# Performance work log

Hardware: AMD Instinct MI355X
Metric: run time of the kernel (lower is better)

The kernel has to match this reference:

```python
import jax, jax.numpy as jnp
import numpy as np

N = 100000      # nodes
E = 1600000     # edges (before self-loops)
IN_DIM = 128
HEADS = 4
C = 32          # hid_dim // heads = 128 // 4
SLOPE = 0.2     # PyG GATConv default negative_slope


def setup_inputs() -> dict:
    key = jax.random.key(0)
    k1, k2, k3, k4, k5 = jax.random.split(key, 5)
    x = jax.random.normal(k1, (N, IN_DIM), dtype=jnp.float32)
    edge_index = jax.random.randint(k2, (2, E), 0, N, dtype=jnp.int32)
    # learned parameters of GATConv
    W = jax.random.normal(k3, (IN_DIM, HEADS * C), dtype=jnp.float32) / np.sqrt(IN_DIM)
    att_src = jax.random.normal(k4, (HEADS, C), dtype=jnp.float32) * 0.1
    att_dst = jax.random.normal(k5, (HEADS, C), dtype=jnp.float32) * 0.1
    bias = jnp.zeros((HEADS * C,), dtype=jnp.float32)
    return {"x": x, "edge_index": edge_index, "W": W,
            "att_src": att_src, "att_dst": att_dst, "bias": bias}


def reference(x, edge_index, W, att_src, att_dst, bias):
    # PyG GATConv default add_self_loops=True
    loops = jnp.arange(N, dtype=edge_index.dtype)
    ei = jnp.concatenate([edge_index, jnp.stack([loops, loops])], axis=1)
    src, dst = ei[0], ei[1]                       # messages flow src -> dst

    h = (x @ W).reshape(N, HEADS, C)              # [N,H,C]
    a_src = jnp.einsum('nhc,hc->nh', h, att_src)  # [N,H]
    a_dst = jnp.einsum('nhc,hc->nh', h, att_dst)  # [N,H]

    e = a_src[src] + a_dst[dst]                   # [E+N,H] per-edge logits
    e = jax.nn.leaky_relu(e, SLOPE)

    # segment softmax over edges sharing a destination node
    m = jax.ops.segment_max(e, dst, num_segments=N)        # [N,H]
    e = jnp.exp(e - m[dst])
    s = jax.ops.segment_sum(e, dst, num_segments=N)        # [N,H]
    alpha = e / (s[dst] + 1e-16)                            # [E+N,H]

    msg = h[src] * alpha[:, :, None]                        # [E+N,H,C]
    out = jax.ops.segment_sum(msg, dst, num_segments=N)     # [N,H,C]
    return out.reshape(N, HEADS * C) + bias                 # concat heads + bias
```

## Files before the change

### kernel.cpp

```cpp
#include <hip/hip_runtime.h>
#include <cstddef>

#define HEADS 4
#define HC 128
#define SLOPE 0.2f
#define NPBUCK 256
#define NSBMAX 512
#define SBCAP 5120
#define CHUNK 4096

using half8 = __attribute__((ext_vector_type(8))) _Float16;
using f32x4 = __attribute__((ext_vector_type(4))) float;

__device__ __forceinline__ float edge_w(float v) {
    v = v > 0.f ? v : SLOPE * v;
    return __expf(v);
}
__device__ __forceinline__ float2 up2(unsigned w) {
    union { unsigned u; _Float16 f[2]; } c; c.u = w;
    return make_float2((float)c.f[0], (float)c.f[1]);
}

__global__ void wt_kernel(const float* __restrict__ W, _Float16* __restrict__ WTh) {
    int k = threadIdx.x;
    int nn = blockIdx.x;
    WTh[nn * HC + k] = (_Float16)W[k * HC + nn];
}

__global__ __launch_bounds__(256)
void gemm_att_count_kernel(const float* __restrict__ x, const _Float16* __restrict__ WTh,
                           const float* __restrict__ att_src, const float* __restrict__ att_dst,
                           _Float16* __restrict__ h2,
                           float* __restrict__ a_s, float* __restrict__ a_d,
                           const int* __restrict__ ei, int* __restrict__ cnt2d,
                           int gb, int E, int n) {
    __shared__ int cnt[NSBMAX];
    int tid = threadIdx.x;

    if (blockIdx.x >= gb) {
        int cb = blockIdx.x - gb;
        for (int i = tid; i < NSBMAX; i += 256) cnt[i] = 0;
        __syncthreads();
        int Etot = E + n;
        int e0 = cb * CHUNK;
        int eend = e0 + CHUNK; if (eend > Etot) eend = Etot;
        for (int e = e0 + tid; e < eend; e += 256) {
            int dst = (e < E) ? ei[E + e] : (e - E);
            atomicAdd(&cnt[dst >> 8], 1);
        }
        __syncthreads();
        int* row = cnt2d + (size_t)cb * NSBMAX;
        for (int i = tid; i < NSBMAX; i += 256) row[i] = cnt[i];
        return;
    }

    int wv   = tid >> 6;
    int lane = tid & 63;
    int t    = lane & 15;
    int q    = lane >> 4;
    int r0   = blockIdx.x * 64 + wv * 16;

    f32x4 acc[8];
#pragma unroll
    for (int ct = 0; ct < 8; ++ct) acc[ct] = (f32x4){0.f, 0.f, 0.f, 0.f};

    int  arow = r0 + t;
    bool aval = arow < n;
    const float* xp = x + (size_t)(aval ? arow : 0) * HC;

    for (int kc = 0; kc < 4; ++kc) {
        int k0 = kc * 32 + q * 8;
        half8 a;
        float4 fa = *(const float4*)(xp + k0);
        float4 fb = *(const float4*)(xp + k0 + 4);
        if (!aval) { fa = make_float4(0.f,0.f,0.f,0.f); fb = fa; }
        a[0] = (_Float16)fa.x; a[1] = (_Float16)fa.y;
        a[2] = (_Float16)fa.z; a[3] = (_Float16)fa.w;
        a[4] = (_Float16)fb.x; a[5] = (_Float16)fb.y;
        a[6] = (_Float16)fb.z; a[7] = (_Float16)fb.w;
#pragma unroll
        for (int ct = 0; ct < 8; ++ct) {
            half8 b = *(const half8*)(WTh + (size_t)(ct * 16 + t) * HC + k0);
            acc[ct] = __builtin_amdgcn_mfma_f32_16x16x32_f16(a, b, acc[ct], 0, 0, 0);
        }
    }

#pragma unroll
    for (int reg = 0; reg < 4; ++reg) {
        int row = r0 + q * 4 + reg;
        if (row < n) {
#pragma unroll
            for (int ct = 0; ct < 8; ++ct)
                h2[(size_t)row * HC + ct * 16 + t] = (_Float16)acc[ct][reg];
        }
    }

    float asv[8], adv[8];
#pragma unroll
    for (int ct = 0; ct < 8; ++ct) {
        asv[ct] = att_src[ct * 16 + t];
        adv[ct] = att_dst[ct * 16 + t];
    }
#pragma unroll
    for (int reg = 0; reg < 4; ++reg) {
        int row = r0 + q * 4 + reg;
        float4 ps, pd;
        ps.x = acc[0][reg]*asv[0] + acc[1][reg]*asv[1];
        ps.y = acc[2][reg]*asv[2] + acc[3][reg]*asv[3];
        ps.z = acc[4][reg]*asv[4] + acc[5][reg]*asv[5];
        ps.w = acc[6][reg]*asv[6] + acc[7][reg]*asv[7];
        pd.x = acc[0][reg]*adv[0] + acc[1][reg]*adv[1];
        pd.y = acc[2][reg]*adv[2] + acc[3][reg]*adv[3];
        pd.z = acc[4][reg]*adv[4] + acc[5][reg]*adv[5];
        pd.w = acc[6][reg]*adv[6] + acc[7][reg]*adv[7];
#pragma unroll
        for (int m = 1; m < 16; m <<= 1) {
            ps.x += __shfl_xor(ps.x, m); ps.y += __shfl_xor(ps.y, m);
            ps.z += __shfl_xor(ps.z, m); ps.w += __shfl_xor(ps.w, m);
            pd.x += __shfl_xor(pd.x, m); pd.y += __shfl_xor(pd.y, m);
            pd.z += __shfl_xor(pd.z, m); pd.w += __shfl_xor(pd.w, m);
        }
        if (t == 0 && row < n) {
            ((float4*)a_s)[row] = ps;
            ((float4*)a_d)[row] = pd;
        }
    }
}

__global__ __launch_bounds__(512)
void colscan_kernel(const int* __restrict__ cnt2d, int* __restrict__ base2d,
                    int* __restrict__ bucketend, int nchunks) {
    __shared__ int tmp[512];
    int b = blockIdx.x;
    int t = threadIdx.x;
    int v = (t < nchunks) ? cnt2d[(size_t)t * NSBMAX + b] : 0;
    tmp[t] = v;
    __syncthreads();
#pragma unroll
    for (int off = 1; off < 512; off <<= 1) {
        int u = (t >= off) ? tmp[t - off] : 0;
        __syncthreads();
        tmp[t] += u;
        __syncthreads();
    }
    if (t < nchunks) base2d[(size_t)t * NSBMAX + b] = b * SBCAP + tmp[t] - v;
    if (t == 511) bucketend[b] = b * SBCAP + tmp[511];
}

__global__ __launch_bounds__(256)
void scatter_kernel(const int* __restrict__ ei, int E, int n,
                    const int* __restrict__ base2d, int2* __restrict__ binned) {
    __shared__ int cur[NSBMAX];
    int tid = threadIdx.x;
    const int* row = base2d + (size_t)blockIdx.x * NSBMAX;
    for (int i = tid; i < NSBMAX; i += 256) cur[i] = row[i];
    __syncthreads();
    int Etot = E + n;
    int e0 = blockIdx.x * CHUNK;
    int eend = e0 + CHUNK; if (eend > Etot) eend = Etot;
    for (int e = e0 + tid; e < eend; e += 256) {
        int src, dst;
        if (e < E) { src = ei[e]; dst = ei[E + e]; }
        else       { src = e - E; dst = src; }
        int p = atomicAdd(&cur[dst >> 8], 1);
        binned[p] = make_int2(src, dst);
    }
}

__global__ __launch_bounds__(256)
void place_kernel(const int* __restrict__ bucketend, const int2* __restrict__ binned,
                  int* __restrict__ sorted, int* __restrict__ rowstart,
                  int* __restrict__ deg, int n) {
    __shared__ int cnt[256];
    __shared__ int pos[256];
    int b = blockIdx.x;
    int dst0 = b << 8;
    int rows = n - dst0; if (rows > 256) rows = 256;
    int tid = threadIdx.x;

    cnt[tid] = 0;
    __syncthreads();
    int wstart = b * SBCAP;
    int wend   = bucketend[b];
    for (int e = wstart + tid; e < wend; e += 256)
        atomicAdd(&cnt[binned[e].y - dst0], 1);
    __syncthreads();

    int d = cnt[tid];
    pos[tid] = d;
    __syncthreads();
#pragma unroll
    for (int off = 1; off < 256; off <<= 1) {
        int v = (tid >= off) ? pos[tid - off] : 0;
        __syncthreads();
        pos[tid] += v;
        __syncthreads();
    }
    int excl = pos[tid] - d;
    if (tid < rows) {
        rowstart[dst0 + tid] = wstart + excl;
        deg[dst0 + tid] = d;
    }
    cnt[tid] = excl;
    __syncthreads();
    for (int e = wstart + tid; e < wend; e += 256) {
        int2 ed = binned[e];
        int p = atomicAdd(&cnt[ed.y - dst0], 1);
        sorted[wstart + p] = ed.x;
    }
}

__global__ __launch_bounds__(256)
void agg_kernel(const int* __restrict__ rowstart, const int* __restrict__ deg,
                const int* __restrict__ sorted,
                const float* __restrict__ a_s, const float* __restrict__ a_d,
                const _Float16* __restrict__ h2, const float* __restrict__ bias,
                float* __restrict__ out, int n) {
    int dst = blockIdx.x * 4 + (threadIdx.x >> 6);
    if (dst >= n) return;
    int lane = threadIdx.x & 63;
    int li   = lane & 15;
    int sub  = lane >> 4;
    int head = li >> 2;
    int start = rowstart[dst];
    int cntv  = deg[dst];

    float ad = a_d[(size_t)dst * 4 + head];
    const uint4* h4 = (const uint4*)h2;
    float acc[8] = {0.f,0.f,0.f,0.f,0.f,0.f,0.f,0.f};
    float wsum = 0.f;

    for (int j = 0; j < cntv; j += 16) {
        int   sv[4]; float wv[4]; uint4 hv[4];
#pragma unroll
        for (int k = 0; k < 4; ++k) {
            int idx = j + k * 4 + sub;
            bool valid = idx < cntv;
            sv[k] = sorted[start + (valid ? idx : cntv - 1)];
            wv[k] = valid ? 1.f : 0.f;
        }
#pragma unroll
        for (int k = 0; k < 4; ++k)
            hv[k] = h4[(size_t)sv[k] * 16 + li];
#pragma unroll
        for (int k = 0; k < 4; ++k) {
            float w = wv[k] * edge_w(a_s[(size_t)sv[k] * 4 + head] + ad);
            float2 f0 = up2(hv[k].x), f1 = up2(hv[k].y),
                   f2 = up2(hv[k].z), f3 = up2(hv[k].w);
            acc[0] = fmaf(w, f0.x, acc[0]); acc[1] = fmaf(w, f0.y, acc[1]);
            acc[2] = fmaf(w, f1.x, acc[2]); acc[3] = fmaf(w, f1.y, acc[3]);
            acc[4] = fmaf(w, f2.x, acc[4]); acc[5] = fmaf(w, f2.y, acc[5]);
            acc[6] = fmaf(w, f3.x, acc[6]); acc[7] = fmaf(w, f3.y, acc[7]);
            wsum += w;
        }
    }

#pragma unroll
    for (int k = 0; k < 8; ++k) {
        acc[k] += __shfl_xor(acc[k], 16);
        acc[k] += __shfl_xor(acc[k], 32);
    }
    wsum += __shfl_xor(wsum, 16);
    wsum += __shfl_xor(wsum, 32);

    if (sub == 0) {
        float inv = 1.f / wsum;
        float4 b0 = ((const float4*)bias)[li * 2];
        float4 b1 = ((const float4*)bias)[li * 2 + 1];
        float4 o0 = make_float4(acc[0]*inv + b0.x, acc[1]*inv + b0.y,
                                acc[2]*inv + b0.z, acc[3]*inv + b0.w);
        float4 o1 = make_float4(acc[4]*inv + b1.x, acc[5]*inv + b1.y,
                                acc[6]*inv + b1.z, acc[7]*inv + b1.w);
        float4* op = (float4*)(out + (size_t)dst * HC);
        op[li * 2]     = o0;
        op[li * 2 + 1] = o1;
    }
}

extern "C" void kernel_launch(void* const* d_in, const int* in_sizes, int n_in,
                              void* d_out, int out_size, void* d_ws, size_t ws_size,
                              hipStream_t stream) {
    const float* x       = (const float*)d_in[0];
    const int*   ei      = (const int*)d_in[1];
    const float* W       = (const float*)d_in[2];
    const float* att_src = (const float*)d_in[3];
    const float* att_dst = (const float*)d_in[4];
    const float* bias    = (const float*)d_in[5];

    int n = in_sizes[0] / HC;
    int E = in_sizes[1] / 2;
    int Etot = E + n;
    int nbuck   = (n + NPBUCK - 1) / NPBUCK;
    int nchunks = (Etot + CHUNK - 1) / CHUNK;
    int gb      = (n + 63) / 64;

    _Float16* h2     = (_Float16*)d_ws;
    _Float16* WTh    = h2 + (size_t)n * HC;
    float* a_s       = (float*)(WTh + HC * HC);
    float* a_d       = a_s + (size_t)n * HEADS;
    int*   cnt2d     = (int*)(a_d + (size_t)n * HEADS);
    int*   base2d    = cnt2d + (size_t)nchunks * NSBMAX;
    int*   bucketend = base2d + (size_t)nchunks * NSBMAX;
    int*   rowstart  = bucketend + NSBMAX;
    int*   deg       = rowstart + n;
    int2*  binned    = (int2*)(deg + n);
    int*   sorted    = (int*)(binned + (size_t)nbuck * SBCAP);
    float* out       = (float*)d_out;

    wt_kernel<<<HC, HC, 0, stream>>>(W, WTh);
    gemm_att_count_kernel<<<gb + nchunks, 256, 0, stream>>>(
        x, WTh, att_src, att_dst, h2, a_s, a_d, ei, cnt2d, gb, E, n);
    colscan_kernel<<<nbuck, 512, 0, stream>>>(cnt2d, base2d, bucketend, nchunks);
    scatter_kernel<<<nchunks, 256, 0, stream>>>(ei, E, n, base2d, binned);
    place_kernel<<<nbuck, 256, 0, stream>>>(bucketend, binned, sorted,
                                            rowstart, deg, n);
    agg_kernel<<<(n + 3) / 4, 256, 0, stream>>>(rowstart, deg, sorted,
                                                a_s, a_d, h2, bias, out, n);
}
```

Before: 264.5 us.

## Assign one 16-lane group per destination node in aggregation kernel

The aggregation kernel now maps each destination node to a 16-thread group instead of a full 64-lane wavefront split into four sub-groups. This drops the cross-sub-group shuffle reduction and the masked writeback, and it packs four destinations per wavefront to cut idle lanes for low-degree nodes (average degree is about 17). The trade-off is that each group walks its edge list serially, four edges per step, so high-degree nodes get less parallelism and there are fewer outstanding gathers per destination.

```diff
diff --git a/kernel.cpp b/kernel.cpp
--- a/kernel.cpp
+++ b/kernel.cpp
@@ -15,10 +15,6 @@
 __device__ __forceinline__ float edge_w(float v) {
     v = v > 0.f ? v : SLOPE * v;
     return __expf(v);
-}
-__device__ __forceinline__ float2 up2(unsigned w) {
-    union { unsigned u; _Float16 f[2]; } c; c.u = w;
-    return make_float2((float)c.f[0], (float)c.f[1]);
 }
 
 __global__ void wt_kernel(const float* __restrict__ W, _Float16* __restrict__ WTh) {
@@ -216,11 +212,9 @@
                 const float* __restrict__ a_s, const float* __restrict__ a_d,
                 const _Float16* __restrict__ h2, const float* __restrict__ bias,
                 float* __restrict__ out, int n) {
-    int dst = blockIdx.x * 4 + (threadIdx.x >> 6);
+    int dst = blockIdx.x * 16 + (threadIdx.x >> 4);
     if (dst >= n) return;
-    int lane = threadIdx.x & 63;
-    int li   = lane & 15;
-    int sub  = lane >> 4;
+    int li   = threadIdx.x & 15;
     int head = li >> 2;
     int start = rowstart[dst];
     int cntv  = deg[dst];
@@ -230,51 +224,44 @@
     float acc[8] = {0.f,0.f,0.f,0.f,0.f,0.f,0.f,0.f};
     float wsum = 0.f;
 
-    for (int j = 0; j < cntv; j += 16) {
-        int   sv[4]; float wv[4]; uint4 hv[4];
+    for (int j = 0; j < cntv; j += 4) {
+        int sv[4]; float wv[4];
 #pragma unroll
         for (int k = 0; k < 4; ++k) {
-            int idx = j + k * 4 + sub;
+            int idx = j + k;
             bool valid = idx < cntv;
-            sv[k] = sorted[start + (valid ? idx : cntv - 1)];
+            sv[k] = sorted[start + (valid ? idx : 0)];
             wv[k] = valid ? 1.f : 0.f;
         }
+        uint4 hv[4];
 #pragma unroll
         for (int k = 0; k < 4; ++k)
             hv[k] = h4[(size_t)sv[k] * 16 + li];
+        float as[4];
+#pragma unroll
+        for (int k = 0; k < 4; ++k)
+            as[k] = a_s[(size_t)sv[k] * 4 + head];
 #pragma unroll
         for (int k = 0; k < 4; ++k) {
-            float w = wv[k] * edge_w(a_s[(size_t)sv[k] * 4 + head] + ad);
-            float2 f0 = up2(hv[k].x), f1 = up2(hv[k].y),
-                   f2 = up2(hv[k].z), f3 = up2(hv[k].w);
-            acc[0] = fmaf(w, f0.x, acc[0]); acc[1] = fmaf(w, f0.y, acc[1]);
-            acc[2] = fmaf(w, f1.x, acc[2]); acc[3] = fmaf(w, f1.y, acc[3]);
-            acc[4] = fmaf(w, f2.x, acc[4]); acc[5] = fmaf(w, f2.y, acc[5]);
-            acc[6] = fmaf(w, f3.x, acc[6]); acc[7] = fmaf(w, f3.y, acc[7]);
+            float w = wv[k] * edge_w(as[k] + ad);
+            union { uint4 u; _Float16 f[8]; } hc; hc.u = hv[k];
+#pragma unroll
+            for (int c = 0; c < 8; ++c)
+                acc[c] = fmaf((float)hc.f[c], w, acc[c]);
             wsum += w;
         }
     }
 
-#pragma unroll
-    for (int k = 0; k < 8; ++k) {
-        acc[k] += __shfl_xor(acc[k], 16);
-        acc[k] += __shfl_xor(acc[k], 32);
-    }
-    wsum += __shfl_xor(wsum, 16);
-    wsum += __shfl_xor(wsum, 32);
-
-    if (sub == 0) {
-        float inv = 1.f / wsum;
-        float4 b0 = ((const float4*)bias)[li * 2];
-        float4 b1 = ((const float4*)bias)[li * 2 + 1];
-        float4 o0 = make_float4(acc[0]*inv + b0.x, acc[1]*inv + b0.y,
-                                acc[2]*inv + b0.z, acc[3]*inv + b0.w);
-        float4 o1 = make_float4(acc[4]*inv + b1.x, acc[5]*inv + b1.y,
-                                acc[6]*inv + b1.z, acc[7]*inv + b1.w);
-        float4* op = (float4*)(out + (size_t)dst * HC);
-        op[li * 2]     = o0;
-        op[li * 2 + 1] = o1;
-    }
+    float inv = 1.f / wsum;
+    float4 b0 = ((const float4*)bias)[li * 2];
+    float4 b1 = ((const float4*)bias)[li * 2 + 1];
+    float4 o0 = make_float4(acc[0]*inv + b0.x, acc[1]*inv + b0.y,
+                            acc[2]*inv + b0.z, acc[3]*inv + b0.w);
+    float4 o1 = make_float4(acc[4]*inv + b1.x, acc[5]*inv + b1.y,
+                            acc[6]*inv + b1.z, acc[7]*inv + b1.w);
+    float4* op = (float4*)(out + (size_t)dst * HC);
+    op[li * 2]     = o0;
+    op[li * 2 + 1] = o1;
 }
 
 extern "C" void kernel_launch(void* const* d_in, const int* in_sizes, int n_in,
@@ -314,6 +301,6 @@
     scatter_kernel<<<nchunks, 256, 0, stream>>>(ei, E, n, base2d, binned);
     place_kernel<<<nbuck, 256, 0, stream>>>(bucketend, binned, sorted,
                                             rowstart, deg, n);
-    agg_kernel<<<(n + 3) / 4, 256, 0, stream>>>(rowstart, deg, sorted,
-                                                a_s, a_d, h2, bias, out, n);
-}
+    agg_kernel<<<(n + 15) / 16, 256, 0, stream>>>(rowstart, deg, sorted,
+                                                  a_s, a_d, h2, bias, out, n);
+}
```

Result: no change. 266.7 us (+0.8%).

## Stage GEMM tiles in swizzled LDS and pack binned edges into one int

Applied to the files above, without the earlier changes.

The projection GEMM now loads a 128-row x tile and the full transposed weight into XOR-swizzled shared memory, and each wave computes two 16-row tiles that share the B fragments. This replaces per-lane global loads of W. Separately, binned edge records are packed as src plus an 8-bit local dst in one int instead of an int2, halving scatter/place traffic. The 64KB of LDS per block also applies to the counting blocks and lowers occupancy. The packing assumes node ids fit in 17 bits.

```diff
diff --git a/kernel.cpp b/kernel.cpp
--- a/kernel.cpp
+++ b/kernel.cpp
@@ -8,6 +8,7 @@
 #define NSBMAX 512
 #define SBCAP 5120
 #define CHUNK 4096
+#define GTILE 128
 
 using half8 = __attribute__((ext_vector_type(8))) _Float16;
 using f32x4 = __attribute__((ext_vector_type(4))) float;
@@ -34,10 +35,12 @@
                            float* __restrict__ a_s, float* __restrict__ a_d,
                            const int* __restrict__ ei, int* __restrict__ cnt2d,
                            int gb, int E, int n) {
-    __shared__ int cnt[NSBMAX];
+    __shared__ _Float16 lA[GTILE * HC];
+    __shared__ _Float16 lB[HC * HC];
     int tid = threadIdx.x;
 
     if (blockIdx.x >= gb) {
+        int* cnt = (int*)lA;
         int cb = blockIdx.x - gb;
         for (int i = tid; i < NSBMAX; i += 256) cnt[i] = 0;
         __syncthreads();
@@ -54,44 +57,53 @@
         return;
     }
 
+    int r0 = blockIdx.x * GTILE;
+#pragma unroll
+    for (int it = 0; it < 16; ++it) {
+        int idx = it * 256 + tid;
+        int r   = idx >> 5;
+        int c8  = idx & 31;
+        int rowg = r0 + r; if (rowg >= n) rowg = n - 1;
+        float4 f = *(const float4*)(x + (size_t)rowg * HC + c8 * 4);
+        union { _Float16 h[4]; uint2 u; } pk;
+        pk.h[0] = (_Float16)f.x; pk.h[1] = (_Float16)f.y;
+        pk.h[2] = (_Float16)f.z; pk.h[3] = (_Float16)f.w;
+        int byte = r * 256 + (((c8 >> 1) ^ (r & 15)) << 4) + ((c8 & 1) << 3);
+        *(uint2*)((char*)lA + byte) = pk.u;
+    }
+#pragma unroll
+    for (int it = 0; it < 8; ++it) {
+        int idx = it * 256 + tid;
+        int r = idx >> 4, c = idx & 15;
+        uint4 v = *(const uint4*)(WTh + (size_t)r * HC + c * 8);
+        *(uint4*)((char*)lB + r * 256 + ((c ^ (r & 15)) << 4)) = v;
+    }
+    __syncthreads();
+
     int wv   = tid >> 6;
     int lane = tid & 63;
     int t    = lane & 15;
     int q    = lane >> 4;
-    int r0   = blockIdx.x * 64 + wv * 16;
-
-    f32x4 acc[8];
-#pragma unroll
-    for (int ct = 0; ct < 8; ++ct) acc[ct] = (f32x4){0.f, 0.f, 0.f, 0.f};
-
-    int  arow = r0 + t;
-    bool aval = arow < n;
-    const float* xp = x + (size_t)(aval ? arow : 0) * HC;
-
+
+    f32x4 acc[2][8];
+#pragma unroll
+    for (int rt = 0; rt < 2; ++rt)
+#pragma unroll
+        for (int ct = 0; ct < 8; ++ct) acc[rt][ct] = (f32x4){0.f, 0.f, 0.f, 0.f};
+
+    int ar0 = wv * 32 + t;
+    int ar1 = ar0 + 16;
+#pragma unroll
     for (int kc = 0; kc < 4; ++kc) {
-        int k0 = kc * 32 + q * 8;
-        half8 a;
-        float4 fa = *(const float4*)(xp + k0);
-        float4 fb = *(const float4*)(xp + k0 + 4);
-        if (!aval) { fa = make_float4(0.f,0.f,0.f,0.f); fb = fa; }
-        a[0] = (_Float16)fa.x; a[1] = (_Float16)fa.y;
-        a[2] = (_Float16)fa.z; a[3] = (_Float16)fa.w;
-        a[4] = (_Float16)fb.x; a[5] = (_Float16)fb.y;
-        a[6] = (_Float16)fb.z; a[7] = (_Float16)fb.w;
+        int c = kc * 4 + q;
+        half8 a0 = *(const half8*)((char*)lA + ar0 * 256 + ((c ^ t) << 4));
+        half8 a1 = *(const half8*)((char*)lA + ar1 * 256 + ((c ^ t) << 4));
 #pragma unroll
         for (int ct = 0; ct < 8; ++ct) {
-            half8 b = *(const half8*)(WTh + (size_t)(ct * 16 + t) * HC + k0);
-            acc[ct] = __builtin_amdgcn_mfma_f32_16x16x32_f16(a, b, acc[ct], 0, 0, 0);
-        }
-    }
-
-#pragma unroll
-    for (int reg = 0; reg < 4; ++reg) {
-        int row = r0 + q * 4 + reg;
-        if (row < n) {
-#pragma unroll
-            for (int ct = 0; ct < 8; ++ct)
-                h2[(size_t)row * HC + ct * 16 + t] = (_Float16)acc[ct][reg];
+            int rb = ct * 16 + t;
+            half8 b = *(const half8*)((char*)lB + rb * 256 + ((c ^ t) << 4));
+            acc[0][ct] = __builtin_amdgcn_mfma_f32_16x16x32_f16(a0, b, acc[0][ct], 0, 0, 0);
+            acc[1][ct] = __builtin_amdgcn_mfma_f32_16x16x32_f16(a1, b, acc[1][ct], 0, 0, 0);
         }
     }
 
@@ -102,27 +114,40 @@
         adv[ct] = att_dst[ct * 16 + t];
     }
 #pragma unroll
-    for (int reg = 0; reg < 4; ++reg) {
-        int row = r0 + q * 4 + reg;
-        float4 ps, pd;
-        ps.x = acc[0][reg]*asv[0] + acc[1][reg]*asv[1];
-        ps.y = acc[2][reg]*asv[2] + acc[3][reg]*asv[3];
-        ps.z = acc[4][reg]*asv[4] + acc[5][reg]*asv[5];
-        ps.w = acc[6][reg]*asv[6] + acc[7][reg]*asv[7];
-        pd.x = acc[0][reg]*adv[0] + acc[1][reg]*adv[1];
-        pd.y = acc[2][reg]*adv[2] + acc[3][reg]*adv[3];
-        pd.z = acc[4][reg]*adv[4] + acc[5][reg]*adv[5];
-        pd.w = acc[6][reg]*adv[6] + acc[7][reg]*adv[7];
-#pragma unroll
-        for (int m = 1; m < 16; m <<= 1) {
-            ps.x += __shfl_xor(ps.x, m); ps.y += __shfl_xor(ps.y, m);
-            ps.z += __shfl_xor(ps.z, m); ps.w += __shfl_xor(ps.w, m);
-            pd.x += __shfl_xor(pd.x, m); pd.y += __shfl_xor(pd.y, m);
-            pd.z += __shfl_xor(pd.z, m); pd.w += __shfl_xor(pd.w, m);
-        }
-        if (t == 0 && row < n) {
-            ((float4*)a_s)[row] = ps;
-            ((float4*)a_d)[row] = pd;
+    for (int rt = 0; rt < 2; ++rt) {
+        int Rbase = r0 + wv * 32 + rt * 16;
+#pragma unroll
+        for (int reg = 0; reg < 4; ++reg) {
+            int row = Rbase + q * 4 + reg;
+            if (row < n) {
+#pragma unroll
+                for (int ct = 0; ct < 8; ++ct)
+                    h2[(size_t)row * HC + ct * 16 + t] = (_Float16)acc[rt][ct][reg];
+            }
+        }
+#pragma unroll
+        for (int reg = 0; reg < 4; ++reg) {
+            int row = Rbase + q * 4 + reg;
+            float4 ps, pd;
+            ps.x = acc[rt][0][reg]*asv[0] + acc[rt][1][reg]*asv[1];
+            ps.y = acc[rt][2][reg]*asv[2] + acc[rt][3][reg]*asv[3];
+            ps.z = acc[rt][4][reg]*asv[4] + acc[rt][5][reg]*asv[5];
+            ps.w = acc[rt][6][reg]*asv[6] + acc[rt][7][reg]*asv[7];
+            pd.x = acc[rt][0][reg]*adv[0] + acc[rt][1][reg]*adv[1];
+            pd.y = acc[rt][2][reg]*adv[2] + acc[rt][3][reg]*adv[3];
+            pd.z = acc[rt][4][reg]*adv[4] + acc[rt][5][reg]*adv[5];
+            pd.w = acc[rt][6][reg]*adv[6] + acc[rt][7][reg]*adv[7];
+#pragma unroll
+            for (int m = 1; m < 16; m <<= 1) {
+                ps.x += __shfl_xor(ps.x, m); ps.y += __shfl_xor(ps.y, m);
+                ps.z += __shfl_xor(ps.z, m); ps.w += __shfl_xor(ps.w, m);
+                pd.x += __shfl_xor(pd.x, m); pd.y += __shfl_xor(pd.y, m);
+                pd.z += __shfl_xor(pd.z, m); pd.w += __shfl_xor(pd.w, m);
+            }
+            if (t == 0 && row < n) {
+                ((float4*)a_s)[row] = ps;
+                ((float4*)a_d)[row] = pd;
+            }
         }
     }
 }
@@ -149,7 +174,7 @@
 
 __global__ __launch_bounds__(256)
 void scatter_kernel(const int* __restrict__ ei, int E, int n,
-                    const int* __restrict__ base2d, int2* __restrict__ binned) {
+                    const int* __restrict__ base2d, int* __restrict__ binned) {
     __shared__ int cur[NSBMAX];
     int tid = threadIdx.x;
     const int* row = base2d + (size_t)blockIdx.x * NSBMAX;
@@ -163,12 +188,12 @@
         if (e < E) { src = ei[e]; dst = ei[E + e]; }
         else       { src = e - E; dst = src; }
         int p = atomicAdd(&cur[dst >> 8], 1);
-        binned[p] = make_int2(src, dst);
+        binned[p] = src | ((dst & 255) << 17);
     }
 }
 
 __global__ __launch_bounds__(256)
-void place_kernel(const int* __restrict__ bucketend, const int2* __restrict__ binned,
+void place_kernel(const int* __restrict__ bucketend, const int* __restrict__ binned,
                   int* __restrict__ sorted, int* __restrict__ rowstart,
                   int* __restrict__ deg, int n) {
     __shared__ int cnt[256];
@@ -183,7 +208,7 @@
     int wstart = b * SBCAP;
     int wend   = bucketend[b];
     for (int e = wstart + tid; e < wend; e += 256)
-        atomicAdd(&cnt[binned[e].y - dst0], 1);
+        atomicAdd(&cnt[binned[e] >> 17], 1);
     __syncthreads();
 
     int d = cnt[tid];
@@ -204,9 +229,9 @@
     cnt[tid] = excl;
     __syncthreads();
     for (int e = wstart + tid; e < wend; e += 256) {
-        int2 ed = binned[e];
-        int p = atomicAdd(&cnt[ed.y - dst0], 1);
-        sorted[wstart + p] = ed.x;
+        int v = binned[e];
+        int p = atomicAdd(&cnt[v >> 17], 1);
+        sorted[wstart + p] = v & 0x1FFFF;
     }
 }
 
@@ -292,7 +317,7 @@
     int Etot = E + n;
     int nbuck   = (n + NPBUCK - 1) / NPBUCK;
     int nchunks = (Etot + CHUNK - 1) / CHUNK;
-    int gb      = (n + 63) / 64;
+    int gb      = (n + GTILE - 1) / GTILE;
 
     _Float16* h2     = (_Float16*)d_ws;
     _Float16* WTh    = h2 + (size_t)n * HC;
@@ -303,8 +328,8 @@
     int*   bucketend = base2d + (size_t)nchunks * NSBMAX;
     int*   rowstart  = bucketend + NSBMAX;
     int*   deg       = rowstart + n;
-    int2*  binned    = (int2*)(deg + n);
-    int*   sorted    = (int*)(binned + (size_t)nbuck * SBCAP);
+    int*   binned    = deg + n;
+    int*   sorted    = binned + (size_t)nbuck * SBCAP;
     float* out       = (float*)d_out;
 
     wt_kernel<<<HC, HC, 0, stream>>>(W, WTh);
```

New measurement: 252.4 us. -4.6%, faster.
